# Kernel tuning notes

Hardware: AMD Instinct MI355X
Metric: run time of the kernel (lower is better)

The kernel has to match this reference:

```python
import jax, jax.numpy as jnp
import numpy as np
import math

D_MODEL, D_FF, N_EXPERTS, TOP_K, N_SHARED = 1024, 4096, 8, 2, 1
B, T = 4, 1024
SCALE = 1.0 / math.sqrt(N_SHARED + TOP_K / N_EXPERTS)


def setup_inputs() -> dict:
    key = jax.random.key(0)
    ks = jax.random.split(key, 10)
    s1 = 1.0 / math.sqrt(D_MODEL)
    s2 = 1.0 / math.sqrt(D_FF)
    return {
        "x": jax.random.normal(ks[0], (B, T, D_MODEL), dtype=jnp.float32),
        "w_router": jax.random.normal(ks[1], (N_EXPERTS, D_MODEL), dtype=jnp.float32) * s1,
        "W1": jax.random.normal(ks[2], (N_EXPERTS, D_FF, D_MODEL), dtype=jnp.float32) * s1,
        "b1": jax.random.normal(ks[3], (N_EXPERTS, D_FF), dtype=jnp.float32) * 0.02,
        "W2": jax.random.normal(ks[4], (N_EXPERTS, D_MODEL, D_FF), dtype=jnp.float32) * s2,
        "b2": jax.random.normal(ks[5], (N_EXPERTS, D_MODEL), dtype=jnp.float32) * 0.02,
        "Ws1": jax.random.normal(ks[6], (D_FF, D_MODEL), dtype=jnp.float32) * s1,
        "bs1": jax.random.normal(ks[7], (D_FF,), dtype=jnp.float32) * 0.02,
        "Ws2": jax.random.normal(ks[8], (D_MODEL, D_FF), dtype=jnp.float32) * s2,
        "bs2": jax.random.normal(ks[9], (D_MODEL,), dtype=jnp.float32) * 0.02,
    }


def reference(x, w_router, W1, b1, W2, b2, Ws1, bs1, Ws2, bs2):
    # Router: logits -> softmax -> top-k gate values (no renormalization, matching source)
    logits = jnp.einsum("btd,ed->bte", x, w_router)      # [B,T,E]
    probs = jax.nn.softmax(logits, axis=-1)
    vals, idx = jax.lax.top_k(probs, TOP_K)               # [B,T,K]
    # Scatter top-k gate values into dense per-expert gates [B,T,E]
    gates = jnp.sum(jax.nn.one_hot(idx, N_EXPERTS, dtype=x.dtype) * vals[..., None], axis=-2)

    # Shared (always-on) expert FFN
    hs = jax.nn.gelu(jnp.einsum("btd,fd->btf", x, Ws1) + bs1)
    acc = jnp.einsum("btf,df->btd", hs, Ws2) + bs2

    # Routed experts, densified combine: sum_e gate[b,t,e] * FFN_e(x[b,t])
    h = jax.nn.gelu(jnp.einsum("btd,efd->btef", x, W1) + b1)   # [B,T,E,F]
    y = jnp.einsum("btef,edf->bted", h, W2) + b2               # [B,T,E,D]
    acc = acc + jnp.einsum("bted,bte->btd", y, gates)

    return SCALE * acc
```

## Files before the change

kernel.cpp:

```cpp
#include <hip/hip_runtime.h>
#include <hip/hip_bf16.h>

#define NTOK 4096
#define DM   1024
#define DF   4096
#define ROWS_TOTAL 12288
#define BM 128
#define BN 128
#define BK 64
#define SCALE_F 0.8944271909999159f
#define PMAX 103

typedef __attribute__((ext_vector_type(8))) short short8;
typedef __attribute__((ext_vector_type(4))) float floatx4;

#define GLD16(gp, lp) __builtin_amdgcn_global_load_lds( \
    (const __attribute__((address_space(1))) void*)(gp), \
    (__attribute__((address_space(3))) void*)(lp), 16, 0, 0)

__device__ __forceinline__ ushort f2bf(float f){
    __hip_bfloat16 h = __float2bfloat16(f);
    return *reinterpret_cast<ushort*>(&h);
}

__device__ __forceinline__ float gelu_tanh(float v){
    float u2 = -1.5957691216057308f * (v + 0.044715f * v * v * v);
    return v / (1.0f + __expf(u2));
}

#define CV8_N0 524288u
#define CV8_N1 4718592u
#define CV8_N2 8912896u
#define CV8_N3 9437184u
#define CV8_N4 9961472u
__global__ __launch_bounds__(256) void cvt_all(
    const float* __restrict__ x,  const float* __restrict__ W1,
    const float* __restrict__ W2, const float* __restrict__ Ws1,
    const float* __restrict__ Ws2,
    ushort* __restrict__ xb,  ushort* __restrict__ w1b, ushort* __restrict__ w2b,
    ushort* __restrict__ ws1b, ushort* __restrict__ ws2b)
{
    unsigned i = blockIdx.x * 256u + threadIdx.x;
    const float* s; ushort* d; unsigned off;
    if      (i < CV8_N0){ s = x;   d = xb;   off = i; }
    else if (i < CV8_N1){ s = W1;  d = w1b;  off = i - CV8_N0; }
    else if (i < CV8_N2){ s = W2;  d = w2b;  off = i - CV8_N1; }
    else if (i < CV8_N3){ s = Ws1; d = ws1b; off = i - CV8_N2; }
    else                { s = Ws2; d = ws2b; off = i - CV8_N3; }
    const float4* s4 = reinterpret_cast<const float4*>(s) + 2 * (size_t)off;
    float4 a = s4[0];
    float4 b = s4[1];
    short8 o;
    o[0] = (short)f2bf(a.x); o[1] = (short)f2bf(a.y);
    o[2] = (short)f2bf(a.z); o[3] = (short)f2bf(a.w);
    o[4] = (short)f2bf(b.x); o[5] = (short)f2bf(b.y);
    o[6] = (short)f2bf(b.z); o[7] = (short)f2bf(b.w);
    reinterpret_cast<short8*>(d)[off] = o;
}

__global__ __launch_bounds__(256) void router_kernel(
    const float* __restrict__ x, const float* __restrict__ wr,
    int* __restrict__ te, float* __restrict__ tg, int* __restrict__ tokarr)
{
    const int token = blockIdx.x * 4 + (threadIdx.x >> 6);
    const int lane  = threadIdx.x & 63;
    const float* xp = x + (size_t)token * DM;
    float s[8];
    #pragma unroll
    for (int e = 0; e < 8; e++) s[e] = 0.f;
    for (int d = lane; d < DM; d += 64){
        float xv = xp[d];
        #pragma unroll
        for (int e = 0; e < 8; e++) s[e] += xv * wr[e * DM + d];
    }
    #pragma unroll
    for (int e = 0; e < 8; e++){
        float v = s[e];
        #pragma unroll
        for (int off = 32; off > 0; off >>= 1) v += __shfl_down(v, off);
        s[e] = v;
    }
    if (lane == 0){
        float m = s[0];
        #pragma unroll
        for (int e = 1; e < 8; e++) m = fmaxf(m, s[e]);
        float p[8]; float sum = 0.f;
        #pragma unroll
        for (int e = 0; e < 8; e++){ p[e] = __expf(s[e] - m); sum += p[e]; }
        float inv = 1.f / sum;
        #pragma unroll
        for (int e = 0; e < 8; e++) p[e] *= inv;
        int i1 = 0; float p1 = p[0];
        #pragma unroll
        for (int e = 1; e < 8; e++) if (p[e] > p1){ p1 = p[e]; i1 = e; }
        int i2 = -1; float p2 = -1.f;
        #pragma unroll
        for (int e = 0; e < 8; e++) if (e != i1 && p[e] > p2){ p2 = p[e]; i2 = e; }
        te[token*2+0] = i1; te[token*2+1] = i2;
        tg[token*2+0] = p1; tg[token*2+1] = p2;
        tokarr[token] = token;
    }
}

__global__ __launch_bounds__(256) void plan_kernel(
    const int* __restrict__ te, int* __restrict__ tokarr,
    int* __restrict__ rowof, int* __restrict__ meta)
{
    __shared__ int lc[9], lcur[9];
    const int t = threadIdx.x;
    if (t < 9) lc[t] = 0;
    __syncthreads();
    for (int j = t; j < NTOK*2; j += 256) atomicAdd(&lc[te[j]], 1);
    __syncthreads();
    if (t == 0){
        int off = NTOK;
        for (int e = 0; e < 8; e++){
            lcur[e]    = off;
            meta[e]    = lc[e];
            meta[16+e] = off;
            meta[32+e] = (lc[e] + BM - 1) / BM;
            off += lc[e];
        }
        meta[8]    = NTOK;
        meta[16+8] = 0;
        meta[32+8] = NTOK / BM;
    }
    __syncthreads();
    for (int j = t; j < NTOK*2; j += 256){
        int e = te[j];
        int p = atomicAdd(&lcur[e], 1);
        tokarr[p] = j >> 1;
        rowof[j]  = p;
    }
}

template<int MODE>
__global__ __launch_bounds__(256) void gemm_kernel(
    const ushort* __restrict__ Abase,
    const ushort* __restrict__ Wb, const ushort* __restrict__ Wsb,
    const float* __restrict__ brout, const float* __restrict__ bsh,
    const int* __restrict__ meta, const int* __restrict__ tokarr,
    ushort* __restrict__ Hout, float* __restrict__ Yout)
{
    const int xcd = blockIdx.x & 7;
    const int q   = blockIdx.x >> 3;
    const int NTG = (MODE == 0) ? 4 : 1;

    int e = -1, r = 0, a0 = 0;
    #pragma unroll
    for (int ee = 0; ee < 9; ee++){
        int w = NTG * meta[32 + ee];
        if (e < 0 && q < a0 + w){ e = ee; r = q - a0; }
        a0 += w;
    }
    if (e < 0) return;
    const int mt_e = meta[32 + e];
    int ntg, mti;
    if (MODE == 0){ ntg = r / mt_e; mti = r - ntg * mt_e; }
    else          { ntg = 0;        mti = r; }
    const int nt   = (MODE == 0) ? (xcd + 8 * ntg) : xcd;
    const int cnt  = meta[e];
    const int base = meta[16 + e];

    const int K = (MODE == 0) ? DM : DF;
    const int N = (MODE == 0) ? DF : DM;
    const ushort* Bp  = (e < 8) ? (Wb + (size_t)e * DF * DM) : Wsb;
    const float* bias = (e < 8) ? (brout + e * N) : bsh;

    __shared__ ushort As[2][BM * BK];
    __shared__ ushort Bs[2][BN * BK];

    const int t    = threadIdx.x;
    const int lane = t & 63;
    const int wv   = t >> 6;
    const int wm   = (wv >> 1) * 64;
    const int wn   = (wv & 1) * 64;
    const int lrow = lane & 15;
    const int quad = lane >> 4;
    const int swz8 = ((lane & 7) ^ (lane >> 3)) * 8;

    const ushort* Ap[4];
    const ushort* Bpp[4];
    ushort* Alds0[4]; ushort* Alds1[4];
    ushort* Blds0[4]; ushort* Blds1[4];
    #pragma unroll
    for (int i = 0; i < 4; i++){
        int rin = wv * 32 + i * 8 + (lane >> 3);
        int pos = mti * BM + rin;
        int clp = (pos < cnt) ? pos : (cnt - 1);
        if (MODE == 0) Ap[i] = Abase + (size_t)tokarr[base + clp] * DM + swz8;
        else           Ap[i] = Abase + (size_t)(base + clp) * DF + swz8;
        Bpp[i]   = Bp + (size_t)(nt * BN + rin) * K + swz8;
        Alds0[i] = &As[0][(wv * 32 + i * 8) * BK];
        Alds1[i] = &As[1][(wv * 32 + i * 8) * BK];
        Blds0[i] = &Bs[0][(wv * 32 + i * 8) * BK];
        Blds1[i] = &Bs[1][(wv * 32 + i * 8) * BK];
    }

    floatx4 acc[4][4];
    #pragma unroll
    for (int mi = 0; mi < 4; mi++)
        #pragma unroll
        for (int ni = 0; ni < 4; ni++)
            acc[mi][ni] = (floatx4){0.f, 0.f, 0.f, 0.f};

    auto compute = [&](const ushort* Asb, const ushort* Bsb){
        #pragma unroll
        for (int kk = 0; kk < BK; kk += 32){
            short8 af[4], bfr[4];
            #pragma unroll
            for (int mi = 0; mi < 4; mi++){
                int row  = wm + mi * 16 + lrow;
                int phys = ((kk >> 3) + quad) ^ (row & 7);
                af[mi] = *reinterpret_cast<const short8*>(&Asb[row * BK + phys * 8]);
            }
            #pragma unroll
            for (int ni = 0; ni < 4; ni++){
                int row  = wn + ni * 16 + lrow;
                int phys = ((kk >> 3) + quad) ^ (row & 7);
                bfr[ni] = *reinterpret_cast<const short8*>(&Bsb[row * BK + phys * 8]);
            }
            #pragma unroll
            for (int mi = 0; mi < 4; mi++)
                #pragma unroll
                for (int ni = 0; ni < 4; ni++)
                    acc[mi][ni] = __builtin_amdgcn_mfma_f32_16x16x32_bf16(af[mi], bfr[ni], acc[mi][ni], 0, 0, 0);
        }
    };

    #pragma unroll
    for (int i = 0; i < 4; i++){
        GLD16(Ap[i], Alds0[i]);
        GLD16(Bpp[i], Blds0[i]);
    }
    asm volatile("s_waitcnt vmcnt(0)" ::: "memory");
    __builtin_amdgcn_s_barrier();

    #pragma unroll 1
    for (int k0 = 0; k0 < K; k0 += 2 * BK){
        #pragma unroll
        for (int i = 0; i < 4; i++){
            GLD16(Ap[i]  + k0 + BK, Alds1[i]);
            GLD16(Bpp[i] + k0 + BK, Blds1[i]);
        }
        compute(As[0], Bs[0]);
        asm volatile("s_waitcnt vmcnt(0)" ::: "memory");
        __builtin_amdgcn_s_barrier();

        if (k0 + 2 * BK < K){
            #pragma unroll
            for (int i = 0; i < 4; i++){
                GLD16(Ap[i]  + k0 + 2 * BK, Alds0[i]);
                GLD16(Bpp[i] + k0 + 2 * BK, Blds0[i]);
            }
        }
        compute(As[1], Bs[1]);
        asm volatile("s_waitcnt vmcnt(0)" ::: "memory");
        __builtin_amdgcn_s_barrier();
    }

    float bv[4];
    #pragma unroll
    for (int ni = 0; ni < 4; ni++) bv[ni] = bias[nt * BN + wn + ni*16 + lrow];

    #pragma unroll
    for (int mi = 0; mi < 4; mi++){
        #pragma unroll
        for (int rg = 0; rg < 4; rg++){
            int s   = wm + mi*16 + quad*4 + rg;
            int pos = mti * BM + s;
            if (pos >= cnt) continue;
            int rr = base + pos;
            if (MODE == 0){
                ushort* hp = Hout + (size_t)rr * DF + nt * BN;
                #pragma unroll
                for (int ni = 0; ni < 4; ni++){
                    float v = acc[mi][ni][rg] + bv[ni];
                    hp[wn + ni*16 + lrow] = f2bf(gelu_tanh(v));
                }
            } else {
                float* yp = Yout + (size_t)rr * DM + nt * BN;
                #pragma unroll
                for (int ni = 0; ni < 4; ni++)
                    yp[wn + ni*16 + lrow] = acc[mi][ni][rg] + bv[ni];
            }
        }
    }
}

__global__ __launch_bounds__(256) void combine_kernel(
    const float* __restrict__ Y, const int* __restrict__ rowof,
    const float* __restrict__ tg, float* __restrict__ out)
{
    const int token = blockIdx.x;
    const int d4    = threadIdx.x;
    const float4* Y4 = reinterpret_cast<const float4*>(Y);
    int r1 = rowof[token*2+0], r2 = rowof[token*2+1];
    float g1 = tg[token*2+0],  g2 = tg[token*2+1];
    float4 a = Y4[(size_t)token * 256 + d4];
    float4 b = Y4[(size_t)r1 * 256 + d4];
    float4 c = Y4[(size_t)r2 * 256 + d4];
    float4 o;
    o.x = SCALE_F * (a.x + g1*b.x + g2*c.x);
    o.y = SCALE_F * (a.y + g1*b.y + g2*c.y);
    o.z = SCALE_F * (a.z + g1*b.z + g2*c.z);
    o.w = SCALE_F * (a.w + g1*b.w + g2*c.w);
    reinterpret_cast<float4*>(out)[(size_t)token * 256 + d4] = o;
}

extern "C" void kernel_launch(void* const* d_in, const int* in_sizes, int n_in,
                              void* d_out, int out_size, void* d_ws, size_t ws_size,
                              hipStream_t stream) {
    const float* x   = (const float*)d_in[0];
    const float* wr  = (const float*)d_in[1];
    const float* W1  = (const float*)d_in[2];
    const float* b1  = (const float*)d_in[3];
    const float* W2  = (const float*)d_in[4];
    const float* b2  = (const float*)d_in[5];
    const float* Ws1 = (const float*)d_in[6];
    const float* bs1 = (const float*)d_in[7];
    const float* Ws2 = (const float*)d_in[8];
    const float* bs2 = (const float*)d_in[9];
    float* out = (float*)d_out;

    char* ws = (char*)d_ws;
    size_t off = 0;
    auto wsalloc = [&](size_t bytes) -> char* {
        char* p = ws + off;
        off += (bytes + 255) & ~(size_t)255;
        return p;
    };
    ushort* xb   = (ushort*)wsalloc((size_t)NTOK * DM * 2);
    ushort* w1b  = (ushort*)wsalloc((size_t)8 * DF * DM * 2);
    ushort* w2b  = (ushort*)wsalloc((size_t)8 * DM * DF * 2);
    ushort* ws1b = (ushort*)wsalloc((size_t)DF * DM * 2);
    ushort* ws2b = (ushort*)wsalloc((size_t)DM * DF * 2);
    ushort* H    = (ushort*)wsalloc((size_t)ROWS_TOTAL * DF * 2);
    int*    tokarr = (int*)wsalloc(ROWS_TOTAL * 4);
    int*    rowof  = (int*)wsalloc(NTOK * 2 * 4);
    int*    te     = (int*)wsalloc(NTOK * 2 * 4);
    float*  tg     = (float*)wsalloc(NTOK * 2 * 4);
    int*    meta   = (int*)wsalloc(64 * 4);
    float*  Y = (float*)w1b;

    cvt_all<<<CV8_N4/256, 256, 0, stream>>>(x, W1, W2, Ws1, Ws2,
                                            xb, w1b, w2b, ws1b, ws2b);
    router_kernel<<<NTOK/4, 256, 0, stream>>>(x, wr, te, tg, tokarr);
    plan_kernel<<<1, 256, 0, stream>>>(te, tokarr, rowof, meta);

    gemm_kernel<0><<<8 * 4 * PMAX, 256, 0, stream>>>(xb, w1b, ws1b, b1, bs1,
        meta, tokarr, H, Y);
    gemm_kernel<1><<<8 * PMAX, 256, 0, stream>>>(H, w2b, ws2b, b2, bs2,
        meta, tokarr, H, Y);

    combine_kernel<<<NTOK, 256, 0, stream>>>(Y, rowof, tg, out);
}
```

Before: 817.0 us.

## Replace double-buffered BK=64 GEMM loop with 4-stage BK=32 LDS pipeline

The GEMM main loop moves from two 64-wide K buffers with full vmcnt(0) waits to four 32-wide K stages, keeping up to three tiles of global-to-LDS loads in flight. Partial vmcnt waits and sched_barriers are meant to overlap memory latency with MFMA work instead of draining all loads every step. The LDS swizzle and load-address mapping are redone for the 32-wide rows. The cost is one barrier per 32-wide K step instead of one per 64, and a more fragile wait-count scheme.

```diff
diff --git a/kernel.cpp b/kernel.cpp
--- a/kernel.cpp
+++ b/kernel.cpp
@@ -7,7 +7,6 @@
 #define ROWS_TOTAL 12288
 #define BM 128
 #define BN 128
-#define BK 64
 #define SCALE_F 0.8944271909999159f
 #define PMAX 103
 
@@ -134,6 +133,42 @@
     }
 }
 
+#define WAIT8 asm volatile("s_waitcnt vmcnt(8)" ::: "memory")
+#define WAIT4 asm volatile("s_waitcnt vmcnt(4)" ::: "memory")
+#define WAIT0 asm volatile("s_waitcnt vmcnt(0)" ::: "memory")
+
+#define ISSUE4(AsX, BsX, ke) do{ \
+    GLD16(ApS0 + (ke), &AsX[(size_t)t * 8]); \
+    GLD16(ApS1 + (ke), &AsX[2048 + (size_t)t * 8]); \
+    GLD16(BpS0 + (ke), &BsX[(size_t)t * 8]); \
+    GLD16(BpS1 + (ke), &BsX[2048 + (size_t)t * 8]); }while(0)
+
+#define COMPUTE32(AsX, BsX) do{ \
+    short8 af[4], bfr[4]; \
+    _Pragma("unroll") \
+    for (int mi = 0; mi < 4; mi++){ \
+        int row = wm + mi * 16 + lrow; \
+        af[mi] = *reinterpret_cast<const short8*>(&AsX[row * 32 + physq]); } \
+    _Pragma("unroll") \
+    for (int ni = 0; ni < 4; ni++){ \
+        int row = wn + ni * 16 + lrow; \
+        bfr[ni] = *reinterpret_cast<const short8*>(&BsX[row * 32 + physq]); } \
+    _Pragma("unroll") \
+    for (int mi = 0; mi < 4; mi++) \
+        _Pragma("unroll") \
+        for (int ni = 0; ni < 4; ni++) \
+            acc[mi][ni] = __builtin_amdgcn_mfma_f32_16x16x32_bf16(af[mi], bfr[ni], acc[mi][ni], 0, 0, 0); \
+    }while(0)
+
+#define STEP(AsC, BsC, AsN, BsN, ke, DOISSUE, WAITM) do{ \
+    WAITM; \
+    __builtin_amdgcn_s_barrier(); \
+    if (DOISSUE) ISSUE4(AsN, BsN, ke); \
+    __builtin_amdgcn_sched_barrier(0); \
+    COMPUTE32(AsC, BsC); \
+    __builtin_amdgcn_sched_barrier(0); \
+}while(0)
+
 template<int MODE>
 __global__ __launch_bounds__(256) void gemm_kernel(
     const ushort* __restrict__ Abase,
@@ -164,11 +199,12 @@
 
     const int K = (MODE == 0) ? DM : DF;
     const int N = (MODE == 0) ? DF : DM;
+    const int ks = K / 32;
     const ushort* Bp  = (e < 8) ? (Wb + (size_t)e * DF * DM) : Wsb;
     const float* bias = (e < 8) ? (brout + e * N) : bsh;
 
-    __shared__ ushort As[2][BM * BK];
-    __shared__ ushort Bs[2][BN * BK];
+    __shared__ __align__(16) ushort As0[BM*32], As1[BM*32], As2[BM*32], As3[BM*32];
+    __shared__ __align__(16) ushort Bs0[BN*32], Bs1[BN*32], Bs2[BN*32], Bs3[BN*32];
 
     const int t    = threadIdx.x;
     const int lane = t & 63;
@@ -177,24 +213,24 @@
     const int wn   = (wv & 1) * 64;
     const int lrow = lane & 15;
     const int quad = lane >> 4;
-    const int swz8 = ((lane & 7) ^ (lane >> 3)) * 8;
-
-    const ushort* Ap[4];
-    const ushort* Bpp[4];
-    ushort* Alds0[4]; ushort* Alds1[4];
-    ushort* Blds0[4]; ushort* Blds1[4];
-    #pragma unroll
-    for (int i = 0; i < 4; i++){
-        int rin = wv * 32 + i * 8 + (lane >> 3);
-        int pos = mti * BM + rin;
-        int clp = (pos < cnt) ? pos : (cnt - 1);
-        if (MODE == 0) Ap[i] = Abase + (size_t)tokarr[base + clp] * DM + swz8;
-        else           Ap[i] = Abase + (size_t)(base + clp) * DF + swz8;
-        Bpp[i]   = Bp + (size_t)(nt * BN + rin) * K + swz8;
-        Alds0[i] = &As[0][(wv * 32 + i * 8) * BK];
-        Alds1[i] = &As[1][(wv * 32 + i * 8) * BK];
-        Blds0[i] = &Bs[0][(wv * 32 + i * 8) * BK];
-        Blds1[i] = &Bs[1][(wv * 32 + i * 8) * BK];
+    const int physq = ((quad ^ (lane & 3)) * 8);
+
+    const int colswz = (((t & 3) ^ ((t >> 2) & 3)) * 8);
+    const ushort *ApS0, *ApS1, *BpS0, *BpS1;
+    {
+        int rin0 = (t >> 2);
+        int rin1 = 64 + (t >> 2);
+        int p0 = mti * BM + rin0; p0 = (p0 < cnt) ? p0 : (cnt - 1);
+        int p1 = mti * BM + rin1; p1 = (p1 < cnt) ? p1 : (cnt - 1);
+        if (MODE == 0){
+            ApS0 = Abase + (size_t)tokarr[base + p0] * DM + colswz;
+            ApS1 = Abase + (size_t)tokarr[base + p1] * DM + colswz;
+        } else {
+            ApS0 = Abase + (size_t)(base + p0) * DF + colswz;
+            ApS1 = Abase + (size_t)(base + p1) * DF + colswz;
+        }
+        BpS0 = Bp + (size_t)(nt * BN + rin0) * K + colswz;
+        BpS1 = Bp + (size_t)(nt * BN + rin1) * K + colswz;
     }
 
     floatx4 acc[4][4];
@@ -204,60 +240,22 @@
         for (int ni = 0; ni < 4; ni++)
             acc[mi][ni] = (floatx4){0.f, 0.f, 0.f, 0.f};
 
-    auto compute = [&](const ushort* Asb, const ushort* Bsb){
-        #pragma unroll
-        for (int kk = 0; kk < BK; kk += 32){
-            short8 af[4], bfr[4];
-            #pragma unroll
-            for (int mi = 0; mi < 4; mi++){
-                int row  = wm + mi * 16 + lrow;
-                int phys = ((kk >> 3) + quad) ^ (row & 7);
-                af[mi] = *reinterpret_cast<const short8*>(&Asb[row * BK + phys * 8]);
-            }
-            #pragma unroll
-            for (int ni = 0; ni < 4; ni++){
-                int row  = wn + ni * 16 + lrow;
-                int phys = ((kk >> 3) + quad) ^ (row & 7);
-                bfr[ni] = *reinterpret_cast<const short8*>(&Bsb[row * BK + phys * 8]);
-            }
-            #pragma unroll
-            for (int mi = 0; mi < 4; mi++)
-                #pragma unroll
-                for (int ni = 0; ni < 4; ni++)
-                    acc[mi][ni] = __builtin_amdgcn_mfma_f32_16x16x32_bf16(af[mi], bfr[ni], acc[mi][ni], 0, 0, 0);
-        }
-    };
-
-    #pragma unroll
-    for (int i = 0; i < 4; i++){
-        GLD16(Ap[i], Alds0[i]);
-        GLD16(Bpp[i], Blds0[i]);
-    }
-    asm volatile("s_waitcnt vmcnt(0)" ::: "memory");
-    __builtin_amdgcn_s_barrier();
+    ISSUE4(As0, Bs0, 0);
+    ISSUE4(As1, Bs1, 32);
+    ISSUE4(As2, Bs2, 64);
 
     #pragma unroll 1
-    for (int k0 = 0; k0 < K; k0 += 2 * BK){
-        #pragma unroll
-        for (int i = 0; i < 4; i++){
-            GLD16(Ap[i]  + k0 + BK, Alds1[i]);
-            GLD16(Bpp[i] + k0 + BK, Blds1[i]);
-        }
-        compute(As[0], Bs[0]);
-        asm volatile("s_waitcnt vmcnt(0)" ::: "memory");
-        __builtin_amdgcn_s_barrier();
-
-        if (k0 + 2 * BK < K){
-            #pragma unroll
-            for (int i = 0; i < 4; i++){
-                GLD16(Ap[i]  + k0 + 2 * BK, Alds0[i]);
-                GLD16(Bpp[i] + k0 + 2 * BK, Blds0[i]);
-            }
-        }
-        compute(As[1], Bs[1]);
-        asm volatile("s_waitcnt vmcnt(0)" ::: "memory");
-        __builtin_amdgcn_s_barrier();
-    }
+    for (int k = 0; k + 8 <= ks; k += 4){
+        const int ke = (k + 3) * 32;
+        STEP(As0, Bs0, As3, Bs3, ke,      true, WAIT8);
+        STEP(As1, Bs1, As0, Bs0, ke + 32, true, WAIT8);
+        STEP(As2, Bs2, As1, Bs1, ke + 64, true, WAIT8);
+        STEP(As3, Bs3, As2, Bs2, ke + 96, true, WAIT8);
+    }
+    STEP(As0, Bs0, As3, Bs3, (ks - 1) * 32, true,  WAIT8);
+    STEP(As1, Bs1, As0, Bs0, 0,             false, WAIT8);
+    STEP(As2, Bs2, As0, Bs0, 0,             false, WAIT4);
+    STEP(As3, Bs3, As0, Bs0, 0,             false, WAIT0);
 
     float bv[4];
     #pragma unroll
```

Measured after the change: 730.9 us. 1.12x faster.
